# Performance work log

Hardware: AMD Instinct MI355X
Metric: run time of the kernel (lower is better)

Reference implementation:

```python
import jax, jax.numpy as jnp
import numpy as np

EPS = 1e-5

def _bn(y, g, b):
    # BatchNorm1d training-mode math: biased batch stats over (batch, spatial)
    m = jnp.mean(y, axis=(0, 2), keepdims=True)
    v = jnp.var(y, axis=(0, 2), keepdims=True)
    return (y - m) / jnp.sqrt(v + EPS) * g[None, :, None] + b[None, :, None]

def setup_inputs() -> dict:
    key = jax.random.key(0)
    ks = jax.random.split(key, 8)
    B, C, HW = 32, 512, 1024
    D = C // 8
    s = 0.02
    return {
        "x": jax.random.normal(ks[0], (B, C, HW), dtype=jnp.float32),
        "bn1_g": jnp.ones((C,), jnp.float32),
        "bn1_b": jnp.zeros((C,), jnp.float32),
        "W_qkv": jax.random.normal(ks[1], (2 * D + C, C), jnp.float32) * s,
        "b_qkv": jnp.zeros((2 * D + C,), jnp.float32),
        "bn2_g": jnp.ones((C,), jnp.float32),
        "bn2_b": jnp.zeros((C,), jnp.float32),
        "W1": jax.random.normal(ks[2], (C, C), jnp.float32) * s,
        "b1": jnp.zeros((C,), jnp.float32),
        "W2": jax.random.normal(ks[3], (C, C), jnp.float32) * s,
        "b2": jnp.zeros((C,), jnp.float32),
    }

def reference(x, bn1_g, bn1_b, W_qkv, b_qkv, bn2_g, bn2_b, W1, b1, W2, b2):
    b, c, hw = x.shape
    d = c // 8
    h = jax.nn.relu(_bn(x, bn1_g, bn1_b))
    # 1x1 conv == channel matmul: [b, 2d+c, hw]
    qkv = jnp.einsum('oc,bch->boh', W_qkv, h) + b_qkv[None, :, None]
    q, k, v = qkv[:, :d], qkv[:, d:2 * d], qkv[:, 2 * d:]
    # beta[b, q_pos, k_pos]; note softmax over axis=1 (query axis), per original
    beta = jnp.einsum('bdq,bdk->bqk', q, k) / jnp.sqrt(jnp.asarray(d, x.dtype))
    beta = jax.nn.softmax(beta, axis=1)
    att = jnp.einsum('bcq,bqk->bck', v, beta)  # [b, c, hw]
    xr = x + att
    y = _bn(xr, bn2_g, bn2_b)
    y = jnp.transpose(y, (0, 2, 1))  # [b, hw, c]
    y = jax.nn.relu(y @ W1.T + b1) @ W2.T + b2
    return xr + jnp.transpose(y, (0, 2, 1))
```

## Files before the change

kernel.cpp:

```cpp
#include <hip/hip_runtime.h>

#define BB 32
#define CC 512
#define HWN 1024
#define DD 64
#define OO 640

typedef short bf16x8 __attribute__((ext_vector_type(8)));
typedef float f32x4 __attribute__((ext_vector_type(4)));
typedef __attribute__((address_space(1))) const void gvoid;
typedef __attribute__((address_space(3))) void svoid;

__device__ __forceinline__ void gload_lds16(const void* g, void* l) {
    __builtin_amdgcn_global_load_lds((gvoid*)g, (svoid*)l, 16, 0, 0);
}

__device__ __forceinline__ unsigned short f2bf(float f) {
    unsigned int u = __float_as_uint(f);
    unsigned int r = u + 0x7FFFu + ((u >> 16) & 1u);
    return (unsigned short)(r >> 16);
}
__device__ __forceinline__ float bf2f(unsigned short h) {
    return __uint_as_float(((unsigned int)h) << 16);
}

__global__ __launch_bounds__(256) void cvt3_kernel(const float* __restrict__ a,
                                                   const float* __restrict__ b,
                                                   const float* __restrict__ c,
                                                   unsigned short* __restrict__ oa,
                                                   unsigned short* __restrict__ ob,
                                                   unsigned short* __restrict__ oc) {
    const int n1 = OO * CC, n2 = CC * CC;
    int i = blockIdx.x * 256 + threadIdx.x;
    if (i < n1)            oa[i] = f2bf(a[i]);
    else if (i < n1 + n2)  ob[i - n1] = f2bf(b[i - n1]);
    else                   oc[i - n1 - n2] = f2bf(c[i - n1 - n2]);
}

template <bool INBF16>
__global__ __launch_bounds__(256) void bn_stats_kernel(const void* __restrict__ xv,
                                                       float* __restrict__ mean,
                                                       float* __restrict__ rstd) {
    int c = blockIdx.x;
    int t = threadIdx.x;
    float s = 0.f, s2 = 0.f;
    if (INBF16) {
        const unsigned int* x = (const unsigned int*)xv;
        for (int b = 0; b < BB; ++b) {
            const unsigned int* p = x + ((size_t)b * CC + c) * (HWN / 2);
#pragma unroll
            for (int i = 0; i < 2; ++i) {
                unsigned int w = p[t + i * 256];
                float v0 = bf2f((unsigned short)(w & 0xffffu));
                float v1 = bf2f((unsigned short)(w >> 16));
                s += v0 + v1; s2 += v0 * v0 + v1 * v1;
            }
        }
    } else {
        const float* x = (const float*)xv;
        for (int b = 0; b < BB; ++b) {
            const float* p = x + ((size_t)b * CC + c) * HWN;
#pragma unroll
            for (int i = 0; i < 4; ++i) {
                float v = p[t + i * 256];
                s += v; s2 += v * v;
            }
        }
    }
    for (int off = 32; off > 0; off >>= 1) {
        s  += __shfl_down(s,  off, 64);
        s2 += __shfl_down(s2, off, 64);
    }
    __shared__ float sh[4], sh2[4];
    int wave = t >> 6;
    if ((t & 63) == 0) { sh[wave] = s; sh2[wave] = s2; }
    __syncthreads();
    if (t == 0) {
        float ts = 0.f, ts2 = 0.f;
        for (int w = 0; w < 4; ++w) { ts += sh[w]; ts2 += sh2[w]; }
        const float invN = 1.f / (float)(BB * HWN);
        float m = ts * invN;
        float var = ts2 * invN - m * m;
        mean[c] = m;
        rstd[c] = rsqrtf(var + 1e-5f);
    }
}

template <bool RELU, bool INBF16>
__global__ __launch_bounds__(256) void bn_apply_t_kernel(const void* __restrict__ xv,
                                                         const float* __restrict__ mean,
                                                         const float* __restrict__ rstd,
                                                         const float* __restrict__ g,
                                                         const float* __restrict__ bta,
                                                         unsigned short* __restrict__ outT) {
    __shared__ float tile[64][65];
    int b  = blockIdx.z;
    int c0 = blockIdx.y * 64;
    int s0 = blockIdx.x * 64;
    int t = threadIdx.x;
    int sl = t & 63, grp = t >> 6;
#pragma unroll
    for (int i = 0; i < 16; ++i) {
        int cr = i * 4 + grp;
        int c = c0 + cr;
        float r  = rstd[c] * g[c];
        float sh = bta[c] - mean[c] * r;
        float xval;
        if (INBF16) {
            const unsigned short* xb = (const unsigned short*)xv;
            xval = bf2f(xb[((size_t)b * CC + c0 + cr) * HWN + s0 + sl]);
        } else {
            const float* xb = (const float*)xv;
            xval = xb[((size_t)b * CC + c0 + cr) * HWN + s0 + sl];
        }
        float v = fmaf(xval, r, sh);
        if (RELU) v = fmaxf(v, 0.f);
        tile[cr][sl] = v;
    }
    __syncthreads();
    unsigned short* ob = outT + ((size_t)b * HWN + s0) * CC + c0;
#pragma unroll
    for (int i = 0; i < 16; ++i) {
        int srow = i * 4 + grp;
        ob[(size_t)srow * CC + sl] = f2bf(tile[sl][srow]);
    }
}

__global__ __launch_bounds__(256) void reduce_invsum_kernel(const float* __restrict__ part,
                                                            float* __restrict__ invsum) {
    int idx = blockIdx.x * 256 + threadIdx.x;
    int b = idx >> 10, k = idx & 1023;
    float s = 0.f;
#pragma unroll
    for (int n = 0; n < 8; ++n) s += part[(((size_t)b * 8 + n) << 10) + k];
    invsum[idx] = 1.f / s;
}

__global__ __launch_bounds__(256) void reduce_bnstats_kernel(const float* __restrict__ part,
                                                             float* __restrict__ mean,
                                                             float* __restrict__ rstd) {
    int c = blockIdx.x * 256 + threadIdx.x;
    float s = 0.f, s2 = 0.f;
    for (int p = 0; p < BB * 8; ++p) {
        s  += part[(size_t)p * 1024 + c];
        s2 += part[(size_t)p * 1024 + 512 + c];
    }
    const float invN = 1.f / (float)(BB * HWN);
    float m = s * invN;
    mean[c] = m;
    rstd[c] = rsqrtf(s2 * invN - m * m + 1e-5f);
}

template <bool OUTBF16, int BIASMODE , bool RELU,
          int RESMODE , int SCALEMODE, int ROWRED>
__global__ __launch_bounds__(256, 4) void mfma_gemm(const unsigned short* __restrict__ A,
                                                 const unsigned short* __restrict__ Bt,
                                                 const float* __restrict__ bias,
                                                 const void* __restrict__ resid,
                                                 void* __restrict__ C,
                                                 int K, int lda, int ldb, int ldc,
                                                 long strideA, long strideB, long strideC,
                                                 float scale,
                                                 const float* __restrict__ cscale, long strideCS,
                                                 float* __restrict__ rowpart) {
    __shared__ __align__(16) unsigned short As[2][128 * 32];
    __shared__ __align__(16) unsigned short Bs[2][128 * 32];
    __shared__ float rsS[2][128];
    __shared__ float rqS[2][128];
    int b  = blockIdx.z;
    int m0 = blockIdx.y * 128;
    int n0 = blockIdx.x * 128;
    const unsigned short* Ab = A  + (size_t)b * strideA;
    const unsigned short* Bb = Bt + (size_t)b * strideB;
    int t = threadIdx.x;
    int wv = t >> 6, L = t & 63;
    int wm = (wv >> 1) * 64, wn = (wv & 1) * 64;
    int lr = L & 15, lq = L >> 4;
    int srow = t >> 2;
    int gchunk = (t & 3) ^ ((t >> 3) & 3);
    int skof = gchunk * 8;
    int swz = (lr >> 1) & 3;

    int aoff[4], boff[4];
#pragma unroll
    for (int i = 0; i < 4; ++i) {
        aoff[i] = (wm + i * 16 + lr) * 32 + ((lq ^ swz) * 8);
        boff[i] = (wn + i * 16 + lr) * 32 + ((lq ^ swz) * 8);
    }

    const unsigned short* gA0 = Ab + (size_t)(m0 + srow) * lda + skof;
    const unsigned short* gA1 = Ab + (size_t)(m0 + 64 + srow) * lda + skof;
    const unsigned short* gB0 = Bb + (size_t)(n0 + srow) * ldb + skof;
    const unsigned short* gB1 = Bb + (size_t)(n0 + 64 + srow) * ldb + skof;

    f32x4 acc[4][4] = {};
    int nIter = K >> 5;

    gload_lds16(gA0, &As[0][t * 8]);
    gload_lds16(gA1, &As[0][64 * 32 + t * 8]);
    gload_lds16(gB0, &Bs[0][t * 8]);
    gload_lds16(gB1, &Bs[0][64 * 32 + t * 8]);

    int p = 0;
    for (int i = 0; i < nIter; ++i) {
        __syncthreads();
        if (i + 1 < nIter) {
            int ko = (i + 1) << 5;
            gload_lds16(gA0 + ko, &As[p ^ 1][t * 8]);
            gload_lds16(gA1 + ko, &As[p ^ 1][64 * 32 + t * 8]);
            gload_lds16(gB0 + ko, &Bs[p ^ 1][t * 8]);
            gload_lds16(gB1 + ko, &Bs[p ^ 1][64 * 32 + t * 8]);
        }
        bf16x8 af[4], bfr[4];
#pragma unroll
        for (int j = 0; j < 4; ++j) af[j]  = *(const bf16x8*)&As[p][aoff[j]];
#pragma unroll
        for (int j = 0; j < 4; ++j) bfr[j] = *(const bf16x8*)&Bs[p][boff[j]];
#pragma unroll
        for (int ii = 0; ii < 4; ++ii)
#pragma unroll
            for (int jj = 0; jj < 4; ++jj)
                acc[ii][jj] = __builtin_amdgcn_mfma_f32_16x16x32_bf16(af[ii], bfr[jj], acc[ii][jj], 0, 0, 0);
        p ^= 1;
    }

    float cs[4];
    if (SCALEMODE == 1) {
#pragma unroll
        for (int j = 0; j < 4; ++j)
            cs[j] = cscale[(size_t)b * strideCS + (n0 + wn + j * 16 + lr)];
    }
#pragma unroll
    for (int i = 0; i < 4; ++i) {
#pragma unroll
        for (int r = 0; r < 4; ++r) {
            int row = m0 + wm + i * 16 + lq * 4 + r;
            float brow = (BIASMODE == 1) ? bias[row] : 0.f;
            float s = 0.f, q2 = 0.f;
#pragma unroll
            for (int j = 0; j < 4; ++j) {
                int col = n0 + wn + j * 16 + lr;
                float v = acc[i][j][r] * scale;
                if (SCALEMODE == 1) v *= cs[j];
                if (BIASMODE == 1) v += brow;
                if (BIASMODE == 2) v += bias[col];
                if (RELU) v = fmaxf(v, 0.f);
                size_t off = (size_t)b * strideC + (size_t)row * ldc + col;
                if (RESMODE == 1) v += ((const float*)resid)[off];
                if (RESMODE == 2) v += bf2f(((const unsigned short*)resid)[off]);
                if (ROWRED == 1) v = __expf(v);
                if (ROWRED) { s += v; if (ROWRED == 2) q2 += v * v; }
                if (OUTBF16) ((unsigned short*)C)[off] = f2bf(v);
                else         ((float*)C)[off] = v;
            }
            if (ROWRED) {
#pragma unroll
                for (int m = 1; m <= 8; m <<= 1) {
                    s += __shfl_xor(s, m, 64);
                    if (ROWRED == 2) q2 += __shfl_xor(q2, m, 64);
                }
                if (lr == 0) {
                    int rl = wm + i * 16 + lq * 4 + r;
                    rsS[wv & 1][rl] = s;
                    if (ROWRED == 2) rqS[wv & 1][rl] = q2;
                }
            }
        }
    }
    if (ROWRED) {
        __syncthreads();
        if (t < 128) {
            int Mtot = gridDim.y << 7;
            size_t base = ((size_t)b * gridDim.x + blockIdx.x) *
                          (size_t)((ROWRED == 2 ? 2 : 1) * Mtot);
            rowpart[base + m0 + t] = rsS[0][t] + rsS[1][t];
            if (ROWRED == 2) rowpart[base + Mtot + m0 + t] = rqS[0][t] + rqS[1][t];
        }
    }
}

extern "C" void kernel_launch(void* const* d_in, const int* in_sizes, int n_in,
                              void* d_out, int out_size, void* d_ws, size_t ws_size,
                              hipStream_t stream) {
    const float* x     = (const float*)d_in[0];
    const float* bn1_g = (const float*)d_in[1];
    const float* bn1_b = (const float*)d_in[2];
    const float* W_qkv = (const float*)d_in[3];
    const float* b_qkv = (const float*)d_in[4];
    const float* bn2_g = (const float*)d_in[5];
    const float* bn2_b = (const float*)d_in[6];
    const float* W1    = (const float*)d_in[7];
    const float* b1    = (const float*)d_in[8];
    const float* W2    = (const float*)d_in[9];
    const float* b2    = (const float*)d_in[10];
    float* out = (float*)d_out;
    char* ws = (char*)d_ws;

    unsigned short* hT    = (unsigned short*)(ws);
    unsigned short* qkT   = (unsigned short*)(ws + 33554432);
    unsigned short* v     = (unsigned short*)(ws + 41943040);
    unsigned short* betaT = (unsigned short*)(ws + 75497472);
    unsigned short* xr    = (unsigned short*)(ws + 142606336);
    unsigned short* Wqkvb = (unsigned short*)(ws + 176160768);
    unsigned short* W1b   = (unsigned short*)(ws + 176816128);
    unsigned short* W2b   = (unsigned short*)(ws + 177340416);
    float* stats = (float*)(ws + 177864704);
    float* mean1 = stats,        *rstd1 = stats + 512;
    float* mean2 = stats + 1024, *rstd2 = stats + 1536;
    unsigned short* ybnT = hT;
    unsigned short* y1T  = v;
    float* rowpartQ  = (float*)(ws);
    float* invsum    = (float*)(ws + 1048576);
    float* rowpartBN = (float*)(ws + 1179648);

    const long sHT = (long)HWN * CC;
    const long sQK = (long)HWN * 128;
    const long sV  = (long)CC * HWN;
    const long sBT = (long)HWN * HWN;

    cvt3_kernel<<<(OO * CC + 2 * CC * CC) / 256, 256, 0, stream>>>(W_qkv, W1, W2, Wqkvb, W1b, W2b);
    bn_stats_kernel<false><<<CC, 256, 0, stream>>>(x, mean1, rstd1);
    bn_apply_t_kernel<true, false><<<dim3(16, 8, BB), 256, 0, stream>>>(x, mean1, rstd1, bn1_g, bn1_b, hT);
    mfma_gemm<true, 2, false, 0, 0, 0><<<dim3(1, 8, BB), 256, 0, stream>>>(
        hT, Wqkvb, b_qkv, nullptr, qkT, 512, 512, 512, 128, sHT, 0, sQK, 1.f, nullptr, 0, nullptr);
    mfma_gemm<true, 1, false, 0, 0, 0><<<dim3(8, 4, BB), 256, 0, stream>>>(
        Wqkvb + 128 * 512, hT, b_qkv + 128, nullptr, v, 512, 512, 512, 1024, 0, sHT, sV, 1.f, nullptr, 0, nullptr);
    mfma_gemm<true, 0, false, 0, 0, 1><<<dim3(8, 8, BB), 256, 0, stream>>>(
        qkT + 64, qkT, nullptr, nullptr, betaT, 64, 128, 128, 1024, sQK, sQK, sBT, 0.125f, nullptr, 0, rowpartQ);
    reduce_invsum_kernel<<<128, 256, 0, stream>>>(rowpartQ, invsum);
    mfma_gemm<true, 0, false, 1, 1, 2><<<dim3(8, 4, BB), 256, 0, stream>>>(
        v, betaT, nullptr, x, xr, 1024, 1024, 1024, 1024, sV, sBT, sV, 1.f, invsum, 1024, rowpartBN);
    reduce_bnstats_kernel<<<2, 256, 0, stream>>>(rowpartBN, mean2, rstd2);
    bn_apply_t_kernel<false, true><<<dim3(16, 8, BB), 256, 0, stream>>>(xr, mean2, rstd2, bn2_g, bn2_b, ybnT);
    mfma_gemm<true, 2, true, 0, 0, 0><<<dim3(4, 8, BB), 256, 0, stream>>>(
        ybnT, W1b, b1, nullptr, y1T, 512, 512, 512, 512, sHT, 0, sHT, 1.f, nullptr, 0, nullptr);
    mfma_gemm<false, 1, false, 2, 0, 0><<<dim3(8, 4, BB), 256, 0, stream>>>(
        W2b, y1T, b2, xr, out, 512, 512, 512, 1024, 0, sHT, sV, 1.f, nullptr, 0, nullptr);
}
```

Measured before the change: 393.6 us.

## Fuse attention score, exp, and PV GEMM into one flash-style kernel

Replaces the separate beta GEMM, the inverse-sum reduction and the PV GEMM with a single kernel. Each block owns 128 key columns and all 512 channels, and loops over query tiles. Per tile it computes QK^T, applies exp, stores the result to LDS as bf16 and accumulates V*E, then normalises by the column sum in the epilogue. This avoids writing and re-reading the 64MB bf16 beta matrix and removes two launches. In exchange the grid is only 256 blocks, each with a large LDS footprint, and no max subtraction is done before exp, matching the prior code.

Result: faster. 376.6 us (-4.3%).

```diff
diff --git a/kernel.cpp b/kernel.cpp
--- a/kernel.cpp
+++ b/kernel.cpp
@@ -126,16 +126,6 @@
     }
 }
 
-__global__ __launch_bounds__(256) void reduce_invsum_kernel(const float* __restrict__ part,
-                                                            float* __restrict__ invsum) {
-    int idx = blockIdx.x * 256 + threadIdx.x;
-    int b = idx >> 10, k = idx & 1023;
-    float s = 0.f;
-#pragma unroll
-    for (int n = 0; n < 8; ++n) s += part[(((size_t)b * 8 + n) << 10) + k];
-    invsum[idx] = 1.f / s;
-}
-
 __global__ __launch_bounds__(256) void reduce_bnstats_kernel(const float* __restrict__ part,
                                                              float* __restrict__ mean,
                                                              float* __restrict__ rstd) {
@@ -151,8 +141,154 @@
     rstd[c] = rsqrtf(s2 * invN - m * m + 1e-5f);
 }
 
+__global__ __launch_bounds__(512, 2) void fused_pv_kernel(
+        const unsigned short* __restrict__ qkTg,
+        const unsigned short* __restrict__ vg,
+        const float* __restrict__ xg,
+        unsigned short* __restrict__ xrg,
+        float* __restrict__ rowpart) {
+    __shared__ __align__(16) unsigned short Ks[2 * 128 * 32];
+    __shared__ __align__(16) unsigned short Qs[2][2 * 64 * 32];
+    __shared__ __align__(16) unsigned short Vs[2 * 512 * 32];
+    __shared__ __align__(16) unsigned short Es[2 * 128 * 32];
+    __shared__ float sS[128];
+    __shared__ float rsS[2][512];
+    __shared__ float rqS[2][512];
+
+    int b = blockIdx.z;
+    int n0 = blockIdx.x * 128;
+    const unsigned short* qk = qkTg + (size_t)b * (HWN * 128);
+    const unsigned short* vb = vg + (size_t)b * ((size_t)CC * HWN);
+    int t = threadIdx.x;
+    int wv = t >> 6, L = t & 63;
+    int lr = L & 15, lq = L >> 4;
+    int swz = (lr >> 1) & 3;
+    int cstrip = (wv >> 1) * 128;
+    int khalf = (wv & 1) * 64;
+
+#pragma unroll
+    for (int is = 0; is < 2; ++is) {
+        int idx = is * 512 + t;
+        int kkd = idx >> 9, row = (idx >> 2) & 127, slot = idx & 3;
+        int ch = slot ^ ((row >> 1) & 3);
+        gload_lds16(qk + (size_t)(n0 + row) * 128 + 64 + kkd * 32 + ch * 8, &Ks[idx * 8]);
+    }
+    {
+        int kkd = t >> 8, row = (t >> 2) & 63, slot = t & 3;
+        int ch = slot ^ ((row >> 1) & 3);
+        gload_lds16(qk + (size_t)row * 128 + kkd * 32 + ch * 8, &Qs[0][t * 8]);
+    }
+
+    f32x4 acc[8][4] = {};
+    float S = 0.f;
+    int p = 0;
+    for (int i = 0; i < 16; ++i) {
+        int q0 = i * 64;
+#pragma unroll
+        for (int is = 0; is < 8; ++is) {
+            int idx = is * 512 + t;
+            int kkq = idx >> 11, row = (idx >> 2) & 511, slot = idx & 3;
+            int ch = slot ^ ((row >> 1) & 3);
+            gload_lds16(vb + (size_t)row * HWN + q0 + kkq * 32 + ch * 8, &Vs[idx * 8]);
+        }
+        if (i + 1 < 16) {
+            int kkd = t >> 8, row = (t >> 2) & 63, slot = t & 3;
+            int ch = slot ^ ((row >> 1) & 3);
+            gload_lds16(qk + (size_t)(q0 + 64 + row) * 128 + kkd * 32 + ch * 8,
+                        &Qs[p ^ 1][t * 8]);
+        }
+        if (i == 0) __syncthreads();
+
+        f32x4 eacc[4] = {};
+#pragma unroll
+        for (int kkd = 0; kkd < 2; ++kkd) {
+            bf16x8 kb = *(const bf16x8*)&Ks[kkd * 4096 + (wv * 16 + lr) * 32 + ((lq ^ swz) * 8)];
+#pragma unroll
+            for (int qi = 0; qi < 4; ++qi) {
+                bf16x8 qa = *(const bf16x8*)&Qs[p][kkd * 2048 + (qi * 16 + lr) * 32 + ((lq ^ swz) * 8)];
+                eacc[qi] = __builtin_amdgcn_mfma_f32_16x16x32_bf16(qa, kb, eacc[qi], 0, 0, 0);
+            }
+        }
+        float spart = 0.f;
+#pragma unroll
+        for (int qi = 0; qi < 4; ++qi) {
+            float e0 = __expf(eacc[qi][0] * 0.125f);
+            float e1 = __expf(eacc[qi][1] * 0.125f);
+            float e2 = __expf(eacc[qi][2] * 0.125f);
+            float e3 = __expf(eacc[qi][3] * 0.125f);
+            spart += (e0 + e1) + (e2 + e3);
+            unsigned int lo = (unsigned int)f2bf(e0) | ((unsigned int)f2bf(e1) << 16);
+            unsigned int hi = (unsigned int)f2bf(e2) | ((unsigned int)f2bf(e3) << 16);
+            int kkq = qi >> 1;
+            int chunkE = (qi & 1) * 2 + (lq >> 1);
+            int addr = kkq * 4096 + (wv * 16 + lr) * 32 + ((chunkE ^ swz) * 8) + (lq & 1) * 4;
+            *(uint2*)&Es[addr] = make_uint2(lo, hi);
+        }
+        spart += __shfl_xor(spart, 16, 64);
+        spart += __shfl_xor(spart, 32, 64);
+        S += spart;
+        __syncthreads();
+
+#pragma unroll
+        for (int kk = 0; kk < 2; ++kk) {
+            bf16x8 af[8], bfj[4];
+#pragma unroll
+            for (int ii = 0; ii < 8; ++ii)
+                af[ii] = *(const bf16x8*)&Vs[kk * 16384 + (cstrip + ii * 16 + lr) * 32 + ((lq ^ swz) * 8)];
+#pragma unroll
+            for (int j = 0; j < 4; ++j)
+                bfj[j] = *(const bf16x8*)&Es[kk * 4096 + (khalf + j * 16 + lr) * 32 + ((lq ^ swz) * 8)];
+#pragma unroll
+            for (int ii = 0; ii < 8; ++ii)
+#pragma unroll
+                for (int j = 0; j < 4; ++j)
+                    acc[ii][j] = __builtin_amdgcn_mfma_f32_16x16x32_bf16(af[ii], bfj[j], acc[ii][j], 0, 0, 0);
+        }
+        __syncthreads();
+        p ^= 1;
+    }
+
+    if (lq == 0) sS[wv * 16 + lr] = S;
+    __syncthreads();
+    float inv[4];
+#pragma unroll
+    for (int j = 0; j < 4; ++j) inv[j] = 1.f / sS[khalf + j * 16 + lr];
+
+    const float* xb = xg + (size_t)b * ((size_t)CC * HWN);
+    unsigned short* xrb = xrg + (size_t)b * ((size_t)CC * HWN);
+#pragma unroll
+    for (int ii = 0; ii < 8; ++ii) {
+#pragma unroll
+        for (int r = 0; r < 4; ++r) {
+            int row = cstrip + ii * 16 + lq * 4 + r;
+            float s = 0.f, q2 = 0.f;
+#pragma unroll
+            for (int j = 0; j < 4; ++j) {
+                int col = n0 + khalf + j * 16 + lr;
+                float val = acc[ii][j][r] * inv[j];
+                size_t off = (size_t)row * HWN + col;
+                val += xb[off];
+                s += val; q2 += val * val;
+                xrb[off] = f2bf(val);
+            }
+#pragma unroll
+            for (int m = 1; m <= 8; m <<= 1) {
+                s += __shfl_xor(s, m, 64);
+                q2 += __shfl_xor(q2, m, 64);
+            }
+            if (lr == 0) { rsS[wv & 1][row] = s; rqS[wv & 1][row] = q2; }
+        }
+    }
+    __syncthreads();
+    {
+        size_t base = ((size_t)b * 8 + blockIdx.x) * 1024;
+        rowpart[base + t] = rsS[0][t] + rsS[1][t];
+        rowpart[base + 512 + t] = rqS[0][t] + rqS[1][t];
+    }
+}
+
 template <bool OUTBF16, int BIASMODE , bool RELU,
-          int RESMODE , int SCALEMODE, int ROWRED>
+          int RESMODE >
 __global__ __launch_bounds__(256, 4) void mfma_gemm(const unsigned short* __restrict__ A,
                                                  const unsigned short* __restrict__ Bt,
                                                  const float* __restrict__ bias,
@@ -160,13 +296,9 @@
                                                  void* __restrict__ C,
                                                  int K, int lda, int ldb, int ldc,
                                                  long strideA, long strideB, long strideC,
-                                                 float scale,
-                                                 const float* __restrict__ cscale, long strideCS,
-                                                 float* __restrict__ rowpart) {
+                                                 float scale) {
     __shared__ __align__(16) unsigned short As[2][128 * 32];
     __shared__ __align__(16) unsigned short Bs[2][128 * 32];
-    __shared__ float rsS[2][128];
-    __shared__ float rqS[2][128];
     int b  = blockIdx.z;
     int m0 = blockIdx.y * 128;
     int n0 = blockIdx.x * 128;
@@ -224,57 +356,25 @@
         p ^= 1;
     }
 
-    float cs[4];
-    if (SCALEMODE == 1) {
-#pragma unroll
-        for (int j = 0; j < 4; ++j)
-            cs[j] = cscale[(size_t)b * strideCS + (n0 + wn + j * 16 + lr)];
-    }
 #pragma unroll
     for (int i = 0; i < 4; ++i) {
 #pragma unroll
         for (int r = 0; r < 4; ++r) {
             int row = m0 + wm + i * 16 + lq * 4 + r;
             float brow = (BIASMODE == 1) ? bias[row] : 0.f;
-            float s = 0.f, q2 = 0.f;
 #pragma unroll
             for (int j = 0; j < 4; ++j) {
                 int col = n0 + wn + j * 16 + lr;
                 float v = acc[i][j][r] * scale;
-                if (SCALEMODE == 1) v *= cs[j];
                 if (BIASMODE == 1) v += brow;
                 if (BIASMODE == 2) v += bias[col];
                 if (RELU) v = fmaxf(v, 0.f);
                 size_t off = (size_t)b * strideC + (size_t)row * ldc + col;
                 if (RESMODE == 1) v += ((const float*)resid)[off];
                 if (RESMODE == 2) v += bf2f(((const unsigned short*)resid)[off]);
-                if (ROWRED == 1) v = __expf(v);
-                if (ROWRED) { s += v; if (ROWRED == 2) q2 += v * v; }
                 if (OUTBF16) ((unsigned short*)C)[off] = f2bf(v);
                 else         ((float*)C)[off] = v;
             }
-            if (ROWRED) {
-#pragma unroll
-                for (int m = 1; m <= 8; m <<= 1) {
-                    s += __shfl_xor(s, m, 64);
-                    if (ROWRED == 2) q2 += __shfl_xor(q2, m, 64);
-                }
-                if (lr == 0) {
-                    int rl = wm + i * 16 + lq * 4 + r;
-                    rsS[wv & 1][rl] = s;
-                    if (ROWRED == 2) rqS[wv & 1][rl] = q2;
-                }
-            }
-        }
-    }
-    if (ROWRED) {
-        __syncthreads();
-        if (t < 128) {
-            int Mtot = gridDim.y << 7;
-            size_t base = ((size_t)b * gridDim.x + blockIdx.x) *
-                          (size_t)((ROWRED == 2 ? 2 : 1) * Mtot);
-            rowpart[base + m0 + t] = rsS[0][t] + rsS[1][t];
-            if (ROWRED == 2) rowpart[base + Mtot + m0 + t] = rqS[0][t] + rqS[1][t];
         }
     }
 }
@@ -299,7 +399,6 @@
     unsigned short* hT    = (unsigned short*)(ws);
     unsigned short* qkT   = (unsigned short*)(ws + 33554432);
     unsigned short* v     = (unsigned short*)(ws + 41943040);
-    unsigned short* betaT = (unsigned short*)(ws + 75497472);
     unsigned short* xr    = (unsigned short*)(ws + 142606336);
     unsigned short* Wqkvb = (unsigned short*)(ws + 176160768);
     unsigned short* W1b   = (unsigned short*)(ws + 176816128);
@@ -309,31 +408,24 @@
     float* mean2 = stats + 1024, *rstd2 = stats + 1536;
     unsigned short* ybnT = hT;
     unsigned short* y1T  = v;
-    float* rowpartQ  = (float*)(ws);
-    float* invsum    = (float*)(ws + 1048576);
     float* rowpartBN = (float*)(ws + 1179648);
 
     const long sHT = (long)HWN * CC;
     const long sQK = (long)HWN * 128;
     const long sV  = (long)CC * HWN;
-    const long sBT = (long)HWN * HWN;
 
     cvt3_kernel<<<(OO * CC + 2 * CC * CC) / 256, 256, 0, stream>>>(W_qkv, W1, W2, Wqkvb, W1b, W2b);
     bn_stats_kernel<false><<<CC, 256, 0, stream>>>(x, mean1, rstd1);
     bn_apply_t_kernel<true, false><<<dim3(16, 8, BB), 256, 0, stream>>>(x, mean1, rstd1, bn1_g, bn1_b, hT);
-    mfma_gemm<true, 2, false, 0, 0, 0><<<dim3(1, 8, BB), 256, 0, stream>>>(
-        hT, Wqkvb, b_qkv, nullptr, qkT, 512, 512, 512, 128, sHT, 0, sQK, 1.f, nullptr, 0, nullptr);
-    mfma_gemm<true, 1, false, 0, 0, 0><<<dim3(8, 4, BB), 256, 0, stream>>>(
-        Wqkvb + 128 * 512, hT, b_qkv + 128, nullptr, v, 512, 512, 512, 1024, 0, sHT, sV, 1.f, nullptr, 0, nullptr);
-    mfma_gemm<true, 0, false, 0, 0, 1><<<dim3(8, 8, BB), 256, 0, stream>>>(
-        qkT + 64, qkT, nullptr, nullptr, betaT, 64, 128, 128, 1024, sQK, sQK, sBT, 0.125f, nullptr, 0, rowpartQ);
-    reduce_invsum_kernel<<<128, 256, 0, stream>>>(rowpartQ, invsum);
-    mfma_gemm<true, 0, false, 1, 1, 2><<<dim3(8, 4, BB), 256, 0, stream>>>(
-        v, betaT, nullptr, x, xr, 1024, 1024, 1024, 1024, sV, sBT, sV, 1.f, invsum, 1024, rowpartBN);
+    mfma_gemm<true, 2, false, 0><<<dim3(1, 8, BB), 256, 0, stream>>>(
+        hT, Wqkvb, b_qkv, nullptr, qkT, 512, 512, 512, 128, sHT, 0, sQK, 1.f);
+    mfma_gemm<true, 1, false, 0><<<dim3(8, 4, BB), 256, 0, stream>>>(
+        Wqkvb + 128 * 512, hT, b_qkv + 128, nullptr, v, 512, 512, 512, 1024, 0, sHT, sV, 1.f);
+    fused_pv_kernel<<<dim3(8, 1, BB), 512, 0, stream>>>(qkT, v, x, xr, rowpartBN);
     reduce_bnstats_kernel<<<2, 256, 0, stream>>>(rowpartBN, mean2, rstd2);
     bn_apply_t_kernel<false, true><<<dim3(16, 8, BB), 256, 0, stream>>>(xr, mean2, rstd2, bn2_g, bn2_b, ybnT);
-    mfma_gemm<true, 2, true, 0, 0, 0><<<dim3(4, 8, BB), 256, 0, stream>>>(
-        ybnT, W1b, b1, nullptr, y1T, 512, 512, 512, 512, sHT, 0, sHT, 1.f, nullptr, 0, nullptr);
-    mfma_gemm<false, 1, false, 2, 0, 0><<<dim3(8, 4, BB), 256, 0, stream>>>(
-        W2b, y1T, b2, xr, out, 512, 512, 512, 1024, 0, sHT, sV, 1.f, nullptr, 0, nullptr);
-}
+    mfma_gemm<true, 2, true, 0><<<dim3(4, 8, BB), 256, 0, stream>>>(
+        ybnT, W1b, b1, nullptr, y1T, 512, 512, 512, 512, sHT, 0, sHT, 1.f);
+    mfma_gemm<false, 1, false, 2><<<dim3(8, 4, BB), 256, 0, stream>>>(
+        W2b, y1T, b2, xr, out, 512, 512, 512, 1024, 0, sHT, sV, 1.f);
+}
```
